# Kernel optimization log

Measured on AMD Instinct MI355X. Metric: run time of the kernel, lower is better.

## Reference

```python
import jax, jax.numpy as jnp
import numpy as np


def setup_inputs() -> dict:
    key = jax.random.key(0)
    ks = jax.random.split(key, 6)
    B, N_IN, N_OUT, C_IN, C_OUT, S, NNZ = 16, 6250, 25000, 64, 64, 9, 75000
    x = jax.random.normal(ks[0], (B, N_IN, C_IN), dtype=jnp.float32)
    trans_values = jax.random.uniform(ks[1], (NNZ,), dtype=jnp.float32)
    trans_row = jax.random.randint(ks[2], (NNZ,), 0, N_OUT, dtype=jnp.int32)
    trans_col = jax.random.randint(ks[3], (NNZ,), 0, N_IN, dtype=jnp.int32)
    spiral_indices = jax.random.randint(ks[4], (N_OUT, S), 0, N_OUT, dtype=jnp.int32)
    # Linear(S*C_IN -> C_OUT), kaiming-ish scale
    W = jax.random.normal(ks[5], (S * C_IN, C_OUT), dtype=jnp.float32) * (1.0 / np.sqrt(S * C_IN))
    b = jnp.zeros((C_OUT,), dtype=jnp.float32)
    return {"x": x, "trans_values": trans_values, "trans_row": trans_row,
            "trans_col": trans_col, "spiral_indices": spiral_indices,
            "W": W, "b": b, "n_out": N_OUT}


def reference(x, trans_values, trans_row, trans_col, spiral_indices, W, b, n_out):
    B, N_in, C = x.shape
    # Pool: gather cols, scale by sparse values, scatter-add to rows
    gathered = x[:, trans_col, :] * trans_values[None, :, None]        # [B, nnz, C]
    pooled = jnp.zeros((B, n_out, C), x.dtype).at[:, trans_row].add(gathered)  # [B, n_out, C]
    # SpiralConv: gather spiral neighborhoods, flatten, linear
    S = spiral_indices.shape[1]
    feat = pooled[:, spiral_indices, :].reshape(B, n_out, S * C)       # [B, n_out, S*C]
    out = feat @ W + b                                                 # [B, n_out, C_out]
    return jax.nn.elu(out)
```

## Files before the change

kernel.cpp:

```cpp
#include <hip/hip_runtime.h>

#define B_     16
#define N_IN_  6250
#define N_OUT_ 25000
#define C_     64
#define S_     9
#define NNZ_   75000
#define MT2_   98

typedef __bf16 bf16x8 __attribute__((ext_vector_type(8)));
typedef float floatx4 __attribute__((ext_vector_type(4)));

__device__ inline void async_copy16(const void* g, void* l) {
    __builtin_amdgcn_global_load_lds(
        (const __attribute__((address_space(1))) void*)g,
        (__attribute__((address_space(3))) void*)l, 16, 0, 0);
}


__global__ void hist_kernel(const int* __restrict__ rows, int* __restrict__ counts, int nnz) {
    int i = blockIdx.x * blockDim.x + threadIdx.x;
    if (i < nnz) atomicAdd(&counts[rows[i]], 1);
}

__global__ void scan1_kernel(const int* __restrict__ counts, int* __restrict__ offsets,
                             int* __restrict__ bsum, int n) {
    __shared__ int wsum[16];
    int t = threadIdx.x;
    int wid = t >> 6, lane = t & 63;
    int i = blockIdx.x * 1024 + t;
    int v = (i < n) ? counts[i] : 0;
    int s = v;
    #pragma unroll
    for (int d = 1; d < 64; d <<= 1) {
        int u = __shfl_up(s, d, 64);
        if (lane >= d) s += u;
    }
    if (lane == 63) wsum[wid] = s;
    __syncthreads();
    if (wid == 0 && lane < 16) {
        int ws = wsum[lane];
        #pragma unroll
        for (int d = 1; d < 16; d <<= 1) {
            int u = __shfl_up(ws, d, 64);
            if (lane >= d) ws += u;
        }
        wsum[lane] = ws;
    }
    __syncthreads();
    int wave_off = (wid == 0) ? 0 : wsum[wid - 1];
    int incl = s + wave_off;
    if (i < n) offsets[i] = incl - v;
    if (t == 1023) bsum[blockIdx.x] = incl;
}

__global__ void scan2_kernel(int* __restrict__ bsum, int* __restrict__ offsets, int nblk, int n) {
    if (threadIdx.x == 0) {
        int t = 0;
        for (int i = 0; i < nblk; ++i) { int v = bsum[i]; bsum[i] = t; t += v; }
        offsets[n] = t;
    }
}

__global__ void scan3_kernel(int* __restrict__ offsets, const int* __restrict__ bsum,
                             int* __restrict__ cursor, int n) {
    int i = blockIdx.x * 1024 + threadIdx.x;
    if (i < n) {
        int o = offsets[i] + bsum[blockIdx.x];
        offsets[i] = o;
        cursor[i] = o;
    }
}

__global__ void fill_kernel(const int* __restrict__ rows, const int* __restrict__ cols,
                            const float* __restrict__ vals, int* __restrict__ cursor,
                            int* __restrict__ ecol, float* __restrict__ eval, int nnz) {
    int i = blockIdx.x * blockDim.x + threadIdx.x;
    if (i < nnz) {
        int p = atomicAdd(&cursor[rows[i]], 1);
        ecol[p] = cols[i];
        eval[p] = vals[i];
    }
}

__global__ __launch_bounds__(256) void pool_kernel(
        const float* __restrict__ x, const int* __restrict__ offsets,
        const int* __restrict__ ecol, const float* __restrict__ eval,
        __bf16* __restrict__ pooled) {
    int t = threadIdx.x;
    int wid = t >> 6, lane = t & 63;
    int row = blockIdx.x * 4 + wid;
    int b = lane >> 2;
    int cq = (lane & 3) << 4;
    int beg = offsets[row], end = offsets[row + 1];

    const float* xb = x + (size_t)b * N_IN_ * C_ + cq;
    floatx4 acc[4] = {};

    int col = 0; float v = 0.f;
    if (beg < end) { col = ecol[beg]; v = eval[beg]; }
    for (int k = beg; k < end; ++k) {
        int col2 = 0; float v2 = 0.f;
        if (k + 1 < end) { col2 = ecol[k + 1]; v2 = eval[k + 1]; }
        const floatx4* xp = reinterpret_cast<const floatx4*>(xb + (size_t)col * C_);
        #pragma unroll
        for (int j = 0; j < 4; ++j) acc[j] += xp[j] * v;
        col = col2; v = v2;
    }

    __bf16* op = pooled + ((size_t)b * N_OUT_ + row) * C_ + cq;
    bf16x8 o0, o1;
    #pragma unroll
    for (int j = 0; j < 4; ++j) {
        o0[j]     = (__bf16)acc[0][j];
        o0[j + 4] = (__bf16)acc[1][j];
        o1[j]     = (__bf16)acc[2][j];
        o1[j + 4] = (__bf16)acc[3][j];
    }
    *reinterpret_cast<bf16x8*>(op)     = o0;
    *reinterpret_cast<bf16x8*>(op + 8) = o1;
}

__global__ void convw_kernel(const float* __restrict__ W, __bf16* __restrict__ WtF) {
    int i = blockIdx.x * blockDim.x + threadIdx.x;
    if (i < 72 * 64 * 8) {
        int kb = i >> 9;
        int n  = (i >> 3) & 63;
        int j  = i & 7;
        WtF[i] = (__bf16)W[(kb * 8 + j) * 64 + n];
    }
}

__global__ __launch_bounds__(256, 2) void gemm_kernel(
        const __bf16* __restrict__ pooled, const int* __restrict__ spiral,
        const __bf16* __restrict__ WtF, const float* __restrict__ bias,
        float* __restrict__ out) {
    __shared__ __bf16 Bs[72 * 64 * 8];

    int bx = blockIdx.x;
    int xcd = bx & 7;
    int rr = bx >> 3;
    int half = (rr >= MT2_) ? 1 : 0;
    int mt = rr - half * MT2_;
    int b = xcd + 8 * half;

    int t = threadIdx.x;
    int wave = t >> 6, lane = t & 63;
    int quad = lane >> 4, l16 = lane & 15;
    int mbase = mt * 256 + wave * 64;

    #pragma unroll
    for (int j = 0; j < 18; ++j) {
        int idx = t + j * 256;
        async_copy16((const char*)WtF + (size_t)idx * 16, (char*)Bs + idx * 16);
    }

    int src[4][S_];
    #pragma unroll
    for (int mi = 0; mi < 4; ++mi) {
        int m = mbase + mi * 16 + l16;
        int mc = (m < N_OUT_) ? m : 0;
        const int* sp = spiral + (size_t)mc * S_;
        int4 a0 = *reinterpret_cast<const int4*>(sp);
        int4 a1 = *reinterpret_cast<const int4*>(sp + 4);
        src[mi][0] = a0.x; src[mi][1] = a0.y; src[mi][2] = a0.z; src[mi][3] = a0.w;
        src[mi][4] = a1.x; src[mi][5] = a1.y; src[mi][6] = a1.z; src[mi][7] = a1.w;
        src[mi][8] = sp[8];
    }
    const __bf16* poolb = pooled + (size_t)b * N_OUT_ * C_;

    __syncthreads();

    floatx4 acc[4][4] = {};
    bf16x8 Acur[4][2], Anxt[4][2];

    auto loadA = [&](int s, bf16x8 (*A)[2]) {
        #pragma unroll
        for (int mi = 0; mi < 4; ++mi) {
            const __bf16* p = poolb + (size_t)src[mi][s] * C_ + quad * 8;
            A[mi][0] = *reinterpret_cast<const bf16x8*>(p);
            A[mi][1] = *reinterpret_cast<const bf16x8*>(p + 32);
        }
    };

    loadA(0, Acur);
    #pragma unroll
    for (int s = 0; s < S_; ++s) {
        if (s + 1 < S_) {
            loadA(s + 1, (s & 1) ? Acur : Anxt);
            __builtin_amdgcn_sched_barrier(0);
        }
        bf16x8 (*A)[2] = (s & 1) ? Anxt : Acur;
        #pragma unroll
        for (int kc = 0; kc < 2; ++kc) {
            #pragma unroll
            for (int nt = 0; nt < 4; ++nt) {
                int kb = s * 8 + kc * 4 + quad;
                bf16x8 bb = *reinterpret_cast<const bf16x8*>(
                    Bs + (((kb << 6) + (nt << 4) + l16) << 3));
                #pragma unroll
                for (int mi = 0; mi < 4; ++mi)
                    acc[mi][nt] = __builtin_amdgcn_mfma_f32_16x16x32_bf16(
                        A[mi][kc], bb, acc[mi][nt], 0, 0, 0);
            }
        }
    }

    float* outb = out + (size_t)b * N_OUT_ * C_;
    #pragma unroll
    for (int mi = 0; mi < 4; ++mi) {
        #pragma unroll
        for (int nt = 0; nt < 4; ++nt) {
            float bn = bias[nt * 16 + l16];
            #pragma unroll
            for (int i = 0; i < 4; ++i) {
                int mm = mbase + mi * 16 + quad * 4 + i;
                if (mm < N_OUT_) {
                    float v = acc[mi][nt][i] + bn;
                    v = (v > 0.0f) ? v : expm1f(v);
                    outb[(size_t)mm * C_ + nt * 16 + l16] = v;
                }
            }
        }
    }
}

extern "C" void kernel_launch(void* const* d_in, const int* in_sizes, int n_in,
                              void* d_out, int out_size, void* d_ws, size_t ws_size,
                              hipStream_t stream) {
    const float* x      = (const float*)d_in[0];
    const float* tvals  = (const float*)d_in[1];
    const int*   trow   = (const int*)d_in[2];
    const int*   tcol   = (const int*)d_in[3];
    const int*   spiral = (const int*)d_in[4];
    const float* W      = (const float*)d_in[5];
    const float* bias   = (const float*)d_in[6];
    float* out = (float*)d_out;

    char* ws = (char*)d_ws;
    size_t off = 0;
    auto alloc = [&](size_t bytes) -> void* {
        void* p = ws + off;
        off += (bytes + 255) & ~(size_t)255;
        return p;
    };
    __bf16* pooled  = (__bf16*)alloc((size_t)B_ * N_OUT_ * C_ * 2);
    __bf16* WtF     = (__bf16*)alloc(72 * 64 * 8 * 2);
    int*    cursor  = (int*)alloc(N_OUT_ * 4);
    int*    offsets = (int*)alloc((N_OUT_ + 1) * 4);
    int*    ecol    = (int*)alloc(NNZ_ * 4);
    float*  eval    = (float*)alloc(NNZ_ * 4);
    int*    counts  = (int*)alloc(N_OUT_ * 4);
    int*    bsum    = (int*)alloc(32 * 4);

    const int NBLK = (N_OUT_ + 1023) / 1024;
    hipMemsetAsync(counts, 0, N_OUT_ * 4, stream);
    hist_kernel<<<(NNZ_ + 255) / 256, 256, 0, stream>>>(trow, counts, NNZ_);
    scan1_kernel<<<NBLK, 1024, 0, stream>>>(counts, offsets, bsum, N_OUT_);
    scan2_kernel<<<1, 64, 0, stream>>>(bsum, offsets, NBLK, N_OUT_);
    scan3_kernel<<<NBLK, 1024, 0, stream>>>(offsets, bsum, cursor, N_OUT_);
    fill_kernel<<<(NNZ_ + 255) / 256, 256, 0, stream>>>(trow, tcol, tvals, cursor, ecol, eval, NNZ_);
    pool_kernel<<<N_OUT_ / 4, 256, 0, stream>>>(x, offsets, ecol, eval, pooled);
    convw_kernel<<<(72 * 64 * 8 + 255) / 256, 256, 0, stream>>>(W, WtF);
    gemm_kernel<<<8 * (2 * MT2_), 256, 0, stream>>>(pooled, spiral, WtF, bias, out);
}
```

Baseline: 288.3 us.

## Merge scan kernels, XCD-aware pool mapping, and enlarge GEMM blocks to 512 threads

Replaces the three-kernel prefix scan with a single-block looping scan, which removes two launches. The pool kernel is remapped so each block handles one XCD-assigned batch pair across 8 rows, with each lane covering 2 channels. This is meant to keep x reads for a batch within one XCD's L2. The GEMM moves to 512-thread blocks covering 512 rows each, with half the W tile copies per thread, trading occupancy per block for fewer tiles. The GEMM body not shown must cope with 8 waves, and 49*512 rows still covers 25000.

```diff
diff --git a/kernel.cpp b/kernel.cpp
--- a/kernel.cpp
+++ b/kernel.cpp
@@ -6,9 +6,10 @@
 #define C_     64
 #define S_     9
 #define NNZ_   75000
-#define MT2_   98
+#define MT3_   49
 
 typedef __bf16 bf16x8 __attribute__((ext_vector_type(8)));
+typedef __bf16 bf16x2 __attribute__((ext_vector_type(2)));
 typedef float floatx4 __attribute__((ext_vector_type(4)));
 
 __device__ inline void async_copy16(const void* g, void* l) {
@@ -23,53 +24,48 @@
     if (i < nnz) atomicAdd(&counts[rows[i]], 1);
 }
 
-__global__ void scan1_kernel(const int* __restrict__ counts, int* __restrict__ offsets,
-                             int* __restrict__ bsum, int n) {
+__global__ __launch_bounds__(1024) void scan_kernel(
+        const int* __restrict__ counts, int* __restrict__ offsets,
+        int* __restrict__ cursor, int n) {
     __shared__ int wsum[16];
+    __shared__ int carry;
     int t = threadIdx.x;
     int wid = t >> 6, lane = t & 63;
-    int i = blockIdx.x * 1024 + t;
-    int v = (i < n) ? counts[i] : 0;
-    int s = v;
-    #pragma unroll
-    for (int d = 1; d < 64; d <<= 1) {
-        int u = __shfl_up(s, d, 64);
-        if (lane >= d) s += u;
-    }
-    if (lane == 63) wsum[wid] = s;
+    if (t == 0) carry = 0;
     __syncthreads();
-    if (wid == 0 && lane < 16) {
-        int ws = wsum[lane];
-        #pragma unroll
-        for (int d = 1; d < 16; d <<= 1) {
-            int u = __shfl_up(ws, d, 64);
-            if (lane >= d) ws += u;
-        }
-        wsum[lane] = ws;
-    }
-    __syncthreads();
-    int wave_off = (wid == 0) ? 0 : wsum[wid - 1];
-    int incl = s + wave_off;
-    if (i < n) offsets[i] = incl - v;
-    if (t == 1023) bsum[blockIdx.x] = incl;
-}
-
-__global__ void scan2_kernel(int* __restrict__ bsum, int* __restrict__ offsets, int nblk, int n) {
-    if (threadIdx.x == 0) {
-        int t = 0;
-        for (int i = 0; i < nblk; ++i) { int v = bsum[i]; bsum[i] = t; t += v; }
-        offsets[n] = t;
-    }
-}
-
-__global__ void scan3_kernel(int* __restrict__ offsets, const int* __restrict__ bsum,
-                             int* __restrict__ cursor, int n) {
-    int i = blockIdx.x * 1024 + threadIdx.x;
-    if (i < n) {
-        int o = offsets[i] + bsum[blockIdx.x];
-        offsets[i] = o;
-        cursor[i] = o;
-    }
+    for (int base = 0; base < n; base += 1024) {
+        int i = base + t;
+        int v = (i < n) ? counts[i] : 0;
+        int s = v;
+        #pragma unroll
+        for (int d = 1; d < 64; d <<= 1) {
+            int u = __shfl_up(s, d, 64);
+            if (lane >= d) s += u;
+        }
+        if (lane == 63) wsum[wid] = s;
+        __syncthreads();
+        if (wid == 0 && lane < 16) {
+            int ws = wsum[lane];
+            #pragma unroll
+            for (int d = 1; d < 16; d <<= 1) {
+                int u = __shfl_up(ws, d, 64);
+                if (lane >= d) ws += u;
+            }
+            wsum[lane] = ws;
+        }
+        __syncthreads();
+        int wave_off = (wid == 0) ? 0 : wsum[wid - 1];
+        int incl = s + wave_off + carry;
+        if (i < n) {
+            int o = incl - v;
+            offsets[i] = o;
+            cursor[i] = o;
+        }
+        __syncthreads();
+        if (t == 1023) carry = incl;
+        __syncthreads();
+    }
+    if (t == 0) offsets[n] = carry;
 }
 
 __global__ void fill_kernel(const int* __restrict__ rows, const int* __restrict__ cols,
@@ -87,38 +83,34 @@
         const float* __restrict__ x, const int* __restrict__ offsets,
         const int* __restrict__ ecol, const float* __restrict__ eval,
         __bf16* __restrict__ pooled) {
+    int bx = blockIdx.x;
+    int xcd = bx & 7;
+    int rg = bx >> 3;
     int t = threadIdx.x;
     int wid = t >> 6, lane = t & 63;
-    int row = blockIdx.x * 4 + wid;
-    int b = lane >> 2;
-    int cq = (lane & 3) << 4;
-    int beg = offsets[row], end = offsets[row + 1];
-
-    const float* xb = x + (size_t)b * N_IN_ * C_ + cq;
-    floatx4 acc[4] = {};
-
-    int col = 0; float v = 0.f;
-    if (beg < end) { col = ecol[beg]; v = eval[beg]; }
-    for (int k = beg; k < end; ++k) {
-        int col2 = 0; float v2 = 0.f;
-        if (k + 1 < end) { col2 = ecol[k + 1]; v2 = eval[k + 1]; }
-        const floatx4* xp = reinterpret_cast<const floatx4*>(xb + (size_t)col * C_);
-        #pragma unroll
-        for (int j = 0; j < 4; ++j) acc[j] += xp[j] * v;
-        col = col2; v = v2;
-    }
-
-    __bf16* op = pooled + ((size_t)b * N_OUT_ + row) * C_ + cq;
-    bf16x8 o0, o1;
-    #pragma unroll
-    for (int j = 0; j < 4; ++j) {
-        o0[j]     = (__bf16)acc[0][j];
-        o0[j + 4] = (__bf16)acc[1][j];
-        o1[j]     = (__bf16)acc[2][j];
-        o1[j + 4] = (__bf16)acc[3][j];
-    }
-    *reinterpret_cast<bf16x8*>(op)     = o0;
-    *reinterpret_cast<bf16x8*>(op + 8) = o1;
+    int b = xcd + 8 * (lane >> 5);
+    int c2 = (lane & 31) * 2;
+    const float* xb = x + (size_t)b * N_IN_ * C_ + c2;
+
+    #pragma unroll
+    for (int r = 0; r < 2; ++r) {
+        int row = rg * 8 + wid * 2 + r;
+        int beg = offsets[row], end = offsets[row + 1];
+        float ax = 0.f, ay = 0.f;
+        int col = 0; float v = 0.f;
+        if (beg < end) { col = ecol[beg]; v = eval[beg]; }
+        for (int k = beg; k < end; ++k) {
+            int col2 = 0; float v2 = 0.f;
+            if (k + 1 < end) { col2 = ecol[k + 1]; v2 = eval[k + 1]; }
+            const float2 xv = *reinterpret_cast<const float2*>(xb + (size_t)col * C_);
+            ax += xv.x * v;
+            ay += xv.y * v;
+            col = col2; v = v2;
+        }
+        bf16x2 o;
+        o[0] = (__bf16)ax; o[1] = (__bf16)ay;
+        *reinterpret_cast<bf16x2*>(pooled + ((size_t)b * N_OUT_ + row) * C_ + c2) = o;
+    }
 }
 
 __global__ void convw_kernel(const float* __restrict__ W, __bf16* __restrict__ WtF) {
@@ -131,7 +123,7 @@
     }
 }
 
-__global__ __launch_bounds__(256, 2) void gemm_kernel(
+__global__ __launch_bounds__(512, 4) void gemm_kernel(
         const __bf16* __restrict__ pooled, const int* __restrict__ spiral,
         const __bf16* __restrict__ WtF, const float* __restrict__ bias,
         float* __restrict__ out) {
@@ -140,18 +132,18 @@
     int bx = blockIdx.x;
     int xcd = bx & 7;
     int rr = bx >> 3;
-    int half = (rr >= MT2_) ? 1 : 0;
-    int mt = rr - half * MT2_;
+    int half = (rr >= MT3_) ? 1 : 0;
+    int mt = rr - half * MT3_;
     int b = xcd + 8 * half;
 
     int t = threadIdx.x;
     int wave = t >> 6, lane = t & 63;
     int quad = lane >> 4, l16 = lane & 15;
-    int mbase = mt * 256 + wave * 64;
-
-    #pragma unroll
-    for (int j = 0; j < 18; ++j) {
-        int idx = t + j * 256;
+    int mbase = mt * 512 + wave * 64;
+
+    #pragma unroll
+    for (int j = 0; j < 9; ++j) {
+        int idx = t + j * 512;
         async_copy16((const char*)WtF + (size_t)idx * 16, (char*)Bs + idx * 16);
     }
 
@@ -251,16 +243,12 @@
     int*    ecol    = (int*)alloc(NNZ_ * 4);
     float*  eval    = (float*)alloc(NNZ_ * 4);
     int*    counts  = (int*)alloc(N_OUT_ * 4);
-    int*    bsum    = (int*)alloc(32 * 4);
-
-    const int NBLK = (N_OUT_ + 1023) / 1024;
+
     hipMemsetAsync(counts, 0, N_OUT_ * 4, stream);
     hist_kernel<<<(NNZ_ + 255) / 256, 256, 0, stream>>>(trow, counts, NNZ_);
-    scan1_kernel<<<NBLK, 1024, 0, stream>>>(counts, offsets, bsum, N_OUT_);
-    scan2_kernel<<<1, 64, 0, stream>>>(bsum, offsets, NBLK, N_OUT_);
-    scan3_kernel<<<NBLK, 1024, 0, stream>>>(offsets, bsum, cursor, N_OUT_);
+    scan_kernel<<<1, 1024, 0, stream>>>(counts, offsets, cursor, N_OUT_);
     fill_kernel<<<(NNZ_ + 255) / 256, 256, 0, stream>>>(trow, tcol, tvals, cursor, ecol, eval, NNZ_);
-    pool_kernel<<<N_OUT_ / 4, 256, 0, stream>>>(x, offsets, ecol, eval, pooled);
     convw_kernel<<<(72 * 64 * 8 + 255) / 256, 256, 0, stream>>>(W, WtF);
-    gemm_kernel<<<8 * (2 * MT2_), 256, 0, stream>>>(pooled, spiral, WtF, bias, out);
-}
+    pool_kernel<<<8 * (N_OUT_ / 8), 256, 0, stream>>>(x, offsets, ecol, eval, pooled);
+    gemm_kernel<<<8 * (2 * MT3_), 512, 0, stream>>>(pooled, spiral, WtF, bias, out);
+}
```

New measurement: 389.8 us. 1.35x slower.
